# Performance work log

Hardware: AMD Instinct MI355X
Metric: run time of the kernel (lower is better)

## Reference

```python
import jax, jax.numpy as jnp
import numpy as np

BATCH, SEQ, DIM = 4, 4096, 256
DT_RANK, D_STATE, NUM_TOKENS = 16, 16, 1024


def _adapool(x, T):
    # uniform window mean == AdaptiveAvgPool1d when S % T == 0
    B, S, D = x.shape
    return x.reshape(B, T, S // T, D).mean(axis=2)


def _layernorm(x, g, b, eps=1e-5):
    mu = x.mean(-1, keepdims=True)
    var = ((x - mu) ** 2).mean(-1, keepdims=True)
    return (x - mu) * jax.lax.rsqrt(var + eps) * g + b


def _gauss_mask(T):
    c = (T + 1) // 2
    idx = jnp.arange(T, dtype=jnp.float32)
    sigma = jnp.abs(idx - c).mean()
    w = jnp.exp(-0.5 * (idx - c) ** 2 / sigma ** 2)
    return w / w.sum()


def _ssm(x, Wdbc, Wdt, bdt, Alog, D):
    A = -jnp.exp(Alog)                                     # (Dm, N)
    dbc = x @ Wdbc.T                                       # (B,L,dt+2N)
    delta = jax.nn.softplus(dbc[..., :DT_RANK] @ Wdt.T + bdt)   # (B,L,Dm)
    Bm = dbc[..., DT_RANK:DT_RANK + D_STATE]               # (B,L,N)
    Cm = dbc[..., DT_RANK + D_STATE:]                      # (B,L,N)
    deltaA = jnp.exp(delta[..., None] * A)                 # (B,L,Dm,N)
    BX = (delta[..., None] * Bm[:, :, None, :]) * x[..., None]
    def comb(c1, c2):
        a1, x1 = c1
        a2, x2 = c2
        return (a2 * a1, a2 * x1 + x2)
    _, hs = jax.lax.associative_scan(comb, (deltaA, BX), axis=1)
    y = jnp.einsum('bldn,bln->bld', hs, Cm) + D * x
    return y


def setup_inputs():
    key = jax.random.key(0)
    ks = jax.random.split(key, 16)
    s = 0.05
    Alog = jnp.tile(jnp.log(jnp.arange(1.0, D_STATE + 1.0, dtype=jnp.float32))[None, :], (DIM, 1))
    return {
        'x': jax.random.normal(ks[0], (BATCH, SEQ, DIM), jnp.float32),
        'ln_g': jnp.ones((DIM,), jnp.float32),
        'ln_b': jnp.zeros((DIM,), jnp.float32),
        'W1': jax.random.normal(ks[1], (DIM, DIM), jnp.float32) * s,
        'b1': jnp.zeros((DIM,), jnp.float32),
        'W2': jax.random.normal(ks[2], (DIM, DIM), jnp.float32) * s,
        'b2': jnp.zeros((DIM,), jnp.float32),
        'Wcf': jax.random.normal(ks[3], (DIM, DIM), jnp.float32) * s,
        'bcf': jnp.zeros((DIM,), jnp.float32),
        'Wcb': jax.random.normal(ks[4], (DIM, DIM), jnp.float32) * s,
        'bcb': jnp.zeros((DIM,), jnp.float32),
        'Wdbc_f': jax.random.normal(ks[5], (DT_RANK + 2 * D_STATE, DIM), jnp.float32) * s,
        'Wdt_f': jax.random.normal(ks[6], (DIM, DT_RANK), jnp.float32) * s,
        'bdt_f': jnp.zeros((DIM,), jnp.float32),
        'Alog_f': Alog,
        'D_f': jnp.ones((DIM,), jnp.float32),
        'Wdbc_b': jax.random.normal(ks[7], (DT_RANK + 2 * D_STATE, DIM), jnp.float32) * s,
        'Wdt_b': jax.random.normal(ks[8], (DIM, DT_RANK), jnp.float32) * s,
        'bdt_b': jnp.zeros((DIM,), jnp.float32),
        'Alog_b': Alog,
        'D_b': jnp.ones((DIM,), jnp.float32),
    }


def reference(x, ln_g, ln_b, W1, b1, W2, b2, Wcf, bcf, Wcb, bcb,
              Wdbc_f, Wdt_f, bdt_f, Alog_f, D_f,
              Wdbc_b, Wdt_b, bdt_b, Alog_b, D_b):
    skip = _adapool(x, NUM_TOKENS)
    xn = _layernorm(x, ln_g, ln_b)
    z = xn @ W1.T + b1
    xp = xn @ W2.T + b2
    mask = _gauss_mask(NUM_TOKENS)[None, :, None]

    # forward direction: 1x1 conv (= channel linear) -> softplus -> SSM
    h1 = jax.nn.softplus(jnp.einsum('bsd,ed->bse', xp, Wcf) + bcf)
    x1 = _ssm(h1, Wdbc_f, Wdt_f, bdt_f, Alog_f, D_f)
    x1 = jax.nn.silu(_adapool(x1, NUM_TOKENS) * mask)

    # backward direction on flipped sequence
    h2 = jax.nn.softplus(jnp.einsum('bsd,ed->bse', xp[:, ::-1], Wcb) + bcb)
    x2 = _ssm(h2, Wdbc_b, Wdt_b, bdt_b, Alog_b, D_b)[:, ::-1]
    x2 = jax.nn.silu(_adapool(x2, NUM_TOKENS) * mask)

    zp = jax.nn.silu(_adapool(z, NUM_TOKENS))
    return zp * x1 + zp * x2 + skip
```

## Files before the change

### kernel.cpp

```cpp
#include <hip/hip_runtime.h>
#include <math.h>


namespace {
constexpr int BB = 4;
constexpr int LL = 4096;
constexpr int DD = 256;
constexpr int NS = 16;
constexpr int NCH = 64;
constexpr int CLEN = 64;
constexpr int TOK = 1024;

constexpr size_t NROW = (size_t)BB * LL;
constexpr size_t NE   = NROW * DD;
constexpr size_t NP   = (size_t)BB * TOK * DD;
constexpr size_t NBC  = NROW * NS;
constexpr size_t NAGG = 2ull * BB * DD * NCH * NS;

constexpr size_t O_XN   = 0;
constexpr size_t O_DLF  = O_XN;
constexpr size_t O_DLB  = NE / 2;
constexpr size_t O_H1X  = NE;
constexpr size_t O_G2X  = NE + NE / 2;
constexpr size_t O_BMF  = 2 * NE;
constexpr size_t O_CMF  = O_BMF + NBC / 2;
constexpr size_t O_BMB  = O_CMF + NBC / 2;
constexpr size_t O_CMB  = O_BMB + NBC / 2;
constexpr size_t O_ZP   = O_CMB + NBC / 2;
constexpr size_t O_SKIP = O_ZP + NP;
constexpr size_t O_Y1   = O_SKIP + NP;
constexpr size_t O_Y2   = O_Y1 + NP;
constexpr size_t O_WF1  = O_Y2 + NP;
constexpr size_t O_BF1  = O_WF1 + 768 * 256 / 2;
constexpr size_t O_WF2F = O_BF1 + 768;
constexpr size_t O_B2F  = O_WF2F + 384 * 256 / 2;
constexpr size_t O_WF2B = O_B2F + 384;
constexpr size_t O_B2B  = O_WF2B + 384 * 256 / 2;
constexpr size_t O_APROD = O_B2B + 384;
constexpr size_t O_HEND = O_APROD + NAGG;
constexpr size_t O_MASK = O_HEND + NAGG;

constexpr int SSTRIDE = 136;
}

typedef __bf16 bf16x8 __attribute__((ext_vector_type(8)));
typedef float f32x4 __attribute__((ext_vector_type(4)));

__device__ __forceinline__ float softplusf(float x) {
    return fmaxf(x, 0.f) + __logf(1.f + __expf(-fabsf(x)));
}
__device__ __forceinline__ float siluf(float x) {
    return x / (1.f + __expf(-x));
}
__device__ __forceinline__ void gl_lds16(const void* g, void* l) {
    __builtin_amdgcn_global_load_lds((const __attribute__((address_space(1))) unsigned int*)g,
                                     (__attribute__((address_space(3))) unsigned int*)l, 16, 0, 0);
}
__device__ __forceinline__ void pow_chain(float e1, float* p) {
    p[0] = e1;
    p[1] = e1 * e1;
    p[2] = p[1] * e1;
    p[3] = p[1] * p[1];
    p[4] = p[3] * p[0];
    p[5] = p[3] * p[1];
    p[6] = p[3] * p[2];
    p[7] = p[3] * p[3];
    p[8]  = p[7] * p[0];
    p[9]  = p[7] * p[1];
    p[10] = p[7] * p[2];
    p[11] = p[7] * p[3];
    p[12] = p[7] * p[4];
    p[13] = p[7] * p[5];
    p[14] = p[7] * p[6];
    p[15] = p[7] * p[7];
}

__global__ __launch_bounds__(256) void prep_all_kernel(
    const float* __restrict__ W1, const float* __restrict__ b1,
    const float* __restrict__ W2, const float* __restrict__ b2,
    const float* __restrict__ Wcf, const float* __restrict__ bcf,
    const float* __restrict__ Wcb, const float* __restrict__ bcb,
    const float* __restrict__ Wdt_f, const float* __restrict__ Wdbc_f, const float* __restrict__ bdt_f,
    const float* __restrict__ Wdt_b, const float* __restrict__ Wdbc_b, const float* __restrict__ bdt_b,
    __bf16* __restrict__ Wf1, float* __restrict__ bf1,
    __bf16* __restrict__ Wf2f, float* __restrict__ b2f,
    __bf16* __restrict__ Wf2b, float* __restrict__ b2b,
    float* __restrict__ mask)
{
    int bx = blockIdx.x, mat = blockIdx.y, k = threadIdx.x;
    if (bx < 256) {
        int j = bx;
        const float* Wc = mat ? Wcb : Wcf;
        float acc = 0.f, accb = 0.f;
        for (int m = 0; m < 256; ++m) {
            float w = Wc[j * 256 + m];
            acc  = fmaf(w, W2[m * 256 + k], acc);
            accb = fmaf(w, b2[m], accb);
        }
        Wf1[(size_t)(256 + mat * 256 + j) * 256 + k] = (__bf16)acc;
        if (k == 0) bf1[256 + mat * 256 + j] = accb + (mat ? bcb[j] : bcf[j]);
        if (mat == 0) {
            Wf1[(size_t)j * 256 + k] = (__bf16)W1[j * 256 + k];
            if (k == 0) bf1[j] = b1[j];
        }
    } else if (bx < 640) {
        int j = bx - 256;
        const float* Wdt  = mat ? Wdt_b : Wdt_f;
        const float* Wdbc = mat ? Wdbc_b : Wdbc_f;
        const float* bdt  = mat ? bdt_b : bdt_f;
        __bf16* Wf2 = mat ? Wf2b : Wf2f;
        float* b2x  = mat ? b2b : b2f;
        float val;
        if (j < 256) {
            float acc = 0.f;
#pragma unroll
            for (int m = 0; m < 16; ++m)
                acc = fmaf(Wdt[j * 16 + m], Wdbc[m * 256 + k], acc);
            val = acc;
        } else if (j < 288) {
            val = Wdbc[(16 + (j - 256)) * 256 + k];
        } else {
            val = 0.f;
        }
        Wf2[(size_t)j * 256 + k] = (__bf16)val;
        if (k == 0) b2x[j] = (j < 256) ? bdt[j] : 0.f;
    } else if (mat == 0) {
        __shared__ float red[4];
        __shared__ float sb;
        float w[4];
        float loc = 0.f;
#pragma unroll
        for (int q = 0; q < 4; ++q) {
            float dd = (float)(k + 256 * q) - 512.f;
            w[q] = __expf(-0.5f * dd * dd * (1.f / 65536.f));
            loc += w[q];
        }
        for (int o = 32; o > 0; o >>= 1) loc += __shfl_xor(loc, o, 64);
        if ((k & 63) == 0) red[k >> 6] = loc;
        __syncthreads();
        if (k == 0) sb = red[0] + red[1] + red[2] + red[3];
        __syncthreads();
        float inv = 1.f / sb;
#pragma unroll
        for (int q = 0; q < 4; ++q) mask[k + 256 * q] = w[q] * inv;
    }
}

__global__ __launch_bounds__(256) void ln_kernel(
    const float* __restrict__ x, const float* __restrict__ lng, const float* __restrict__ lnb,
    __bf16* __restrict__ xn, float* __restrict__ skipo)
{
    __shared__ float red[8];
    __shared__ float mv[2];
    int t = threadIdx.x;
    int r0 = blockIdx.x * 4;
    float gg = lng[t], bbv = lnb[t];
    float acc = 0.f;
    for (int i = 0; i < 4; ++i) {
        size_t r = r0 + i;
        float v = x[r * 256 + t];
        float s = v, q = v * v;
        for (int o = 32; o > 0; o >>= 1) { s += __shfl_xor(s, o, 64); q += __shfl_xor(q, o, 64); }
        if ((t & 63) == 0) { red[t >> 6] = s; red[4 + (t >> 6)] = q; }
        __syncthreads();
        if (t == 0) {
            float S = red[0] + red[1] + red[2] + red[3];
            float Q = red[4] + red[5] + red[6] + red[7];
            float mu = S * (1.f / 256.f);
            mv[0] = mu;
            mv[1] = rsqrtf(Q * (1.f / 256.f) - mu * mu + 1e-5f);
        }
        __syncthreads();
        xn[r * 256 + t] = (__bf16)((v - mv[0]) * mv[1] * gg + bbv);
        acc += v;
        __syncthreads();
    }
    int b = r0 >> 12;
    int g = (r0 & 4095) >> 2;
    skipo[((size_t)b * TOK + g) * 256 + t] = acc * 0.25f;
}

__global__ __launch_bounds__(256) void gemm1_mfma(
    const __bf16* __restrict__ A, const __bf16* __restrict__ Bw, const float* __restrict__ bias,
    float* __restrict__ zp, __bf16* __restrict__ h1x, __bf16* __restrict__ g2x)
{
    __shared__ __align__(16) __bf16 As[4096];
    __shared__ __align__(16) __bf16 Bs[4096];
    __shared__ __align__(16) unsigned char Stage[128 * SSTRIDE * 2];
    int tid = threadIdx.x;
    int lane = tid & 63, wv = tid >> 6;
    int wr = wv >> 1, wc = wv & 1;
    int lm = lane & 15, lq = lane >> 4;
    int m0 = blockIdx.x << 7, n0 = blockIdx.y << 7;

    const __bf16* ga0 = A  + (size_t)(m0 + wv * 32 + lm) * 256 + lq * 8;
    const __bf16* ga1 = ga0 + 16 * 256;
    const __bf16* gb0 = Bw + (size_t)(n0 + wv * 32 + lm) * 256 + lq * 8;
    const __bf16* gb1 = gb0 + 16 * 256;
    __bf16* la0 = &As[(wv * 2    ) * 512];
    __bf16* la1 = &As[(wv * 2 + 1) * 512];
    __bf16* lb0 = &Bs[(wv * 2    ) * 512];
    __bf16* lb1 = &Bs[(wv * 2 + 1) * 512];

    f32x4 acc[4][4];
#pragma unroll
    for (int i = 0; i < 4; ++i)
#pragma unroll
        for (int j = 0; j < 4; ++j) acc[i][j] = 0;

    for (int k0 = 0; k0 < 256; k0 += 32) {
        __syncthreads();
        gl_lds16(ga0 + k0, la0);
        gl_lds16(ga1 + k0, la1);
        gl_lds16(gb0 + k0, lb0);
        gl_lds16(gb1 + k0, lb1);
        __syncthreads();
        bf16x8 af[4], bfr[4];
#pragma unroll
        for (int i = 0; i < 4; ++i)
            af[i] = *(const bf16x8*)&As[(wr * 4 + i) * 512 + lane * 8];
#pragma unroll
        for (int j = 0; j < 4; ++j)
            bfr[j] = *(const bf16x8*)&Bs[(wc * 4 + j) * 512 + lane * 8];
#pragma unroll
        for (int i = 0; i < 4; ++i)
#pragma unroll
            for (int j = 0; j < 4; ++j)
                acc[i][j] = __builtin_amdgcn_mfma_f32_16x16x32_bf16(af[i], bfr[j], acc[i][j], 0, 0, 0);
    }

    int target = blockIdx.y >> 1;
    int colbase = (blockIdx.y & 1) * 128;
    __syncthreads();
    if (target == 0) {
        float* zs = (float*)Stage;
#pragma unroll
        for (int j = 0; j < 4; ++j) {
            int coll = wc * 64 + j * 16 + lm;
            float bv = bias[n0 + coll];
#pragma unroll
            for (int i = 0; i < 4; ++i) {
                int gl = wr * 16 + i * 4 + lq;
                float s = acc[i][j][0] + acc[i][j][1] + acc[i][j][2] + acc[i][j][3];
                zs[gl * 132 + coll] = siluf(0.25f * s + bv);
            }
        }
        __syncthreads();
        int b = m0 >> 12, g0 = (m0 & 4095) >> 2;
        int rl = tid >> 5;
        int c4 = (tid & 31) * 4;
#pragma unroll
        for (int p = 0; p < 4; ++p) {
            int g = p * 8 + rl;
            float4 v = *(float4*)&zs[g * 132 + c4];
            *(float4*)&zp[((size_t)b * TOK + g0 + g) * 256 + colbase + c4] = v;
        }
    } else {
        __bf16* hs = (__bf16*)Stage;
#pragma unroll
        for (int j = 0; j < 4; ++j) {
            int coll = wc * 64 + j * 16 + lm;
            float bv = bias[n0 + coll];
#pragma unroll
            for (int i = 0; i < 4; ++i) {
                int rl = wr * 64 + i * 16 + lq * 4;
#pragma unroll
                for (int r = 0; r < 4; ++r)
                    hs[(rl + r) * SSTRIDE + coll] = (__bf16)softplusf(acc[i][j][r] + bv);
            }
        }
        __syncthreads();
        __bf16* outp = (target == 1) ? h1x : g2x;
        int rl = tid >> 4;
        int c8 = (tid & 15) * 8;
#pragma unroll
        for (int p = 0; p < 8; ++p) {
            int row = p * 16 + rl;
            bf16x8 v = *(bf16x8*)&hs[row * SSTRIDE + c8];
            *(bf16x8*)&outp[(size_t)(m0 + row) * 256 + colbase + c8] = v;
        }
    }
}

__global__ __launch_bounds__(256) void gemm2_mfma(
    const __bf16* __restrict__ h1x, const __bf16* __restrict__ g2x,
    const __bf16* __restrict__ Wf, const float* __restrict__ bf2,
    const __bf16* __restrict__ Wb, const float* __restrict__ bb2,
    __bf16* __restrict__ dlf, __bf16* __restrict__ dlb,
    __bf16* __restrict__ BmF, __bf16* __restrict__ CmF,
    __bf16* __restrict__ BmB, __bf16* __restrict__ CmB)
{
    __shared__ __align__(16) __bf16 As[4096];
    __shared__ __align__(16) __bf16 Bs[4096];
    __shared__ __align__(16) unsigned char Stage[128 * SSTRIDE * 2];
    int tid = threadIdx.x;
    int lane = tid & 63, wv = tid >> 6;
    int wr = wv >> 1, wc = wv & 1;
    int lm = lane & 15, lq = lane >> 4;
    int m0 = blockIdx.x << 7, n0 = blockIdx.y << 7;
    int dir = blockIdx.z;
    const __bf16* A    = dir ? g2x : h1x;
    const __bf16* Bw   = dir ? Wb : Wf;
    const float* bias  = dir ? bb2 : bf2;
    __bf16* dl = dir ? dlb : dlf;
    __bf16* Bm = dir ? BmB : BmF;
    __bf16* Cm = dir ? CmB : CmF;

    const __bf16* ga0 = A  + (size_t)(m0 + wv * 32 + lm) * 256 + lq * 8;
    const __bf16* ga1 = ga0 + 16 * 256;
    const __bf16* gb0 = Bw + (size_t)(n0 + wv * 32 + lm) * 256 + lq * 8;
    const __bf16* gb1 = gb0 + 16 * 256;
    __bf16* la0 = &As[(wv * 2    ) * 512];
    __bf16* la1 = &As[(wv * 2 + 1) * 512];
    __bf16* lb0 = &Bs[(wv * 2    ) * 512];
    __bf16* lb1 = &Bs[(wv * 2 + 1) * 512];

    f32x4 acc[4][4];
#pragma unroll
    for (int i = 0; i < 4; ++i)
#pragma unroll
        for (int j = 0; j < 4; ++j) acc[i][j] = 0;

    for (int k0 = 0; k0 < 256; k0 += 32) {
        __syncthreads();
        gl_lds16(ga0 + k0, la0);
        gl_lds16(ga1 + k0, la1);
        gl_lds16(gb0 + k0, lb0);
        gl_lds16(gb1 + k0, lb1);
        __syncthreads();
        bf16x8 af[4], bfr[4];
#pragma unroll
        for (int i = 0; i < 4; ++i)
            af[i] = *(const bf16x8*)&As[(wr * 4 + i) * 512 + lane * 8];
#pragma unroll
        for (int j = 0; j < 4; ++j)
            bfr[j] = *(const bf16x8*)&Bs[(wc * 4 + j) * 512 + lane * 8];
#pragma unroll
        for (int i = 0; i < 4; ++i)
#pragma unroll
            for (int j = 0; j < 4; ++j)
                acc[i][j] = __builtin_amdgcn_mfma_f32_16x16x32_bf16(af[i], bfr[j], acc[i][j], 0, 0, 0);
    }

    __syncthreads();
    if (blockIdx.y < 2) {
        __bf16* hs = (__bf16*)Stage;
        int colbase = (blockIdx.y & 1) * 128;
#pragma unroll
        for (int j = 0; j < 4; ++j) {
            int coll = wc * 64 + j * 16 + lm;
            float bv = bias[n0 + coll];
#pragma unroll
            for (int i = 0; i < 4; ++i) {
                int rl = wr * 64 + i * 16 + lq * 4;
#pragma unroll
                for (int r = 0; r < 4; ++r)
                    hs[(rl + r) * SSTRIDE + coll] = (__bf16)softplusf(acc[i][j][r] + bv);
            }
        }
        __syncthreads();
        int rl = tid >> 4;
        int c8 = (tid & 15) * 8;
#pragma unroll
        for (int p = 0; p < 8; ++p) {
            int row = p * 16 + rl;
            bf16x8 v = *(bf16x8*)&hs[row * SSTRIDE + c8];
            *(bf16x8*)&dl[(size_t)(m0 + row) * 256 + colbase + c8] = v;
        }
    } else {
        __bf16* bs_ = (__bf16*)Stage;
        __bf16* cs_ = (__bf16*)Stage + 128 * 24;
        if (wc == 0) {
#pragma unroll
            for (int j = 0; j < 2; ++j) {
                int coll = j * 16 + lm;
                float bv = bias[n0 + coll];
                __bf16* dst = j ? cs_ : bs_;
#pragma unroll
                for (int i = 0; i < 4; ++i) {
                    int rl = wr * 64 + i * 16 + lq * 4;
#pragma unroll
                    for (int r = 0; r < 4; ++r)
                        dst[(rl + r) * 24 + lm] = (__bf16)(acc[i][j][r] + bv);
                }
            }
        }
        __syncthreads();
        int row = tid >> 1;
        int c8 = (tid & 1) * 8;
        bf16x8 vb = *(bf16x8*)&bs_[row * 24 + c8];
        bf16x8 vc = *(bf16x8*)&cs_[row * 24 + c8];
        *(bf16x8*)&Bm[(size_t)(m0 + row) * 16 + c8] = vb;
        *(bf16x8*)&Cm[(size_t)(m0 + row) * 16 + c8] = vc;
    }
}

__global__ __launch_bounds__(256) void scan1_kernel(
    const __bf16* __restrict__ df, const __bf16* __restrict__ db,
    const __bf16* __restrict__ xf, const __bf16* __restrict__ xb,
    const __bf16* __restrict__ bmf, const __bf16* __restrict__ bmb,
    const float* __restrict__ alogf, const float* __restrict__ alogb,
    float* __restrict__ aprod, float* __restrict__ hend)
{
    int d = threadIdx.x;
    int c = blockIdx.x, b = blockIdx.y, dir = blockIdx.z;
    const __bf16* delta = dir ? db : df;
    const __bf16* xin   = dir ? xb : xf;
    const __bf16* Bm    = dir ? bmb : bmf;
    const float* Alog   = dir ? alogb : alogf;

    float A[16];
    bool intOK = true;
#pragma unroll
    for (int n = 0; n < 16; ++n) {
        A[n] = -__expf(Alog[(size_t)d * 16 + n]);
        intOK = intOK && (fabsf(A[n] + (float)(n + 1)) < 1e-3f);
    }
    float h[16];
#pragma unroll
    for (int n = 0; n < 16; ++n) h[n] = 0.f;
    float sd = 0.f;
    int base = c * CLEN;
    if (intOK) {
        for (int it = 0; it < CLEN; ++it) {
            int t = dir ? (base + CLEN - 1 - it) : (base + it);
            size_t row = (size_t)b * LL + t;
            float dlt = (float)delta[row * DD + d];
            float xv  = (float)xin[row * DD + d];
            float common = dlt * xv;
            sd += dlt;
            float p[16];
            pow_chain(__expf(-dlt), p);
            const bf16x8* Bp = (const bf16x8*)&Bm[row * NS];
            bf16x8 b0 = Bp[0], b1 = Bp[1];
#pragma unroll
            for (int n = 0; n < 8; ++n) {
                h[n]     = fmaf(p[n],     h[n],     common * (float)b0[n]);
                h[n + 8] = fmaf(p[n + 8], h[n + 8], common * (float)b1[n]);
            }
        }
        float pe[16];
        pow_chain(__expf(-sd), pe);
        size_t idx = ((((size_t)dir * BB + b) * DD + d) * NCH + c) * NS;
#pragma unroll
        for (int q = 0; q < 4; ++q) {
            float4 av, hv;
            av.x = pe[q * 4 + 0]; av.y = pe[q * 4 + 1]; av.z = pe[q * 4 + 2]; av.w = pe[q * 4 + 3];
            hv.x = h[q * 4 + 0];  hv.y = h[q * 4 + 1];  hv.z = h[q * 4 + 2];  hv.w = h[q * 4 + 3];
            *(float4*)&aprod[idx + q * 4] = av;
            *(float4*)&hend[idx + q * 4] = hv;
        }
    } else {
        for (int it = 0; it < CLEN; ++it) {
            int t = dir ? (base + CLEN - 1 - it) : (base + it);
            size_t row = (size_t)b * LL + t;
            float dlt = (float)delta[row * DD + d];
            float xv  = (float)xin[row * DD + d];
            float common = dlt * xv;
            sd += dlt;
            const bf16x8* Bp = (const bf16x8*)&Bm[row * NS];
            bf16x8 b0 = Bp[0], b1 = Bp[1];
#pragma unroll
            for (int n = 0; n < 8; ++n) {
                h[n]     = fmaf(__expf(dlt * A[n]),     h[n],     common * (float)b0[n]);
                h[n + 8] = fmaf(__expf(dlt * A[n + 8]), h[n + 8], common * (float)b1[n]);
            }
        }
        size_t idx = ((((size_t)dir * BB + b) * DD + d) * NCH + c) * NS;
#pragma unroll
        for (int n = 0; n < 16; ++n) {
            aprod[idx + n] = __expf(sd * A[n]);
            hend[idx + n] = h[n];
        }
    }
}

__global__ __launch_bounds__(256) void scan2_kernel(
    const float* __restrict__ aprod, float* __restrict__ hh)
{
    int g = blockIdx.x * 256 + threadIdx.x;
    int n = g & 15, d = (g >> 4) & 255, b = (g >> 12) & 3, dir = (g >> 14) & 1;
    size_t bidx = (((size_t)dir * BB + b) * DD + d) * NCH;
    float s = 0.f;
    if (!dir) {
#pragma unroll 8
        for (int c = 0; c < NCH; ++c) {
            size_t idx = (bidx + c) * NS + n;
            float a = aprod[idx], he = hh[idx];
            hh[idx] = s;
            s = fmaf(a, s, he);
        }
    } else {
#pragma unroll 8
        for (int c = NCH - 1; c >= 0; --c) {
            size_t idx = (bidx + c) * NS + n;
            float a = aprod[idx], he = hh[idx];
            hh[idx] = s;
            s = fmaf(a, s, he);
        }
    }
}

__global__ __launch_bounds__(256) void scan3_kernel(
    const __bf16* __restrict__ df, const __bf16* __restrict__ db,
    const __bf16* __restrict__ xf, const __bf16* __restrict__ xb,
    const __bf16* __restrict__ bmf, const __bf16* __restrict__ bmb,
    const __bf16* __restrict__ cmf, const __bf16* __restrict__ cmb,
    const float* __restrict__ alogf, const float* __restrict__ alogb,
    const float* __restrict__ Dfp, const float* __restrict__ Dbp,
    const float* __restrict__ hin,
    float* __restrict__ y1, float* __restrict__ y2)
{
    int d = threadIdx.x;
    int c = blockIdx.x, b = blockIdx.y, dir = blockIdx.z;
    const __bf16* delta = dir ? db : df;
    const __bf16* xin   = dir ? xb : xf;
    const __bf16* Bm    = dir ? bmb : bmf;
    const __bf16* Cm    = dir ? cmb : cmf;
    const float* Alog   = dir ? alogb : alogf;
    const float* Dv     = dir ? Dbp : Dfp;
    float* yout = dir ? y2 : y1;

    float A[16];
    bool intOK = true;
#pragma unroll
    for (int n = 0; n < 16; ++n) {
        A[n] = -__expf(Alog[(size_t)d * 16 + n]);
        intOK = intOK && (fabsf(A[n] + (float)(n + 1)) < 1e-3f);
    }
    float Dd = Dv[d];
    float h[16];
    size_t idx = ((((size_t)dir * BB + b) * DD + d) * NCH + c) * NS;
#pragma unroll
    for (int q = 0; q < 4; ++q) {
        float4 hv = *(const float4*)&hin[idx + q * 4];
        h[q * 4 + 0] = hv.x; h[q * 4 + 1] = hv.y; h[q * 4 + 2] = hv.z; h[q * 4 + 3] = hv.w;
    }
    int base = c * CLEN;
    float pool = 0.f;
    if (intOK) {
        for (int it = 0; it < CLEN; ++it) {
            int t = dir ? (base + CLEN - 1 - it) : (base + it);
            size_t row = (size_t)b * LL + t;
            float dlt = (float)delta[row * DD + d];
            float xv  = (float)xin[row * DD + d];
            float common = dlt * xv;
            float p[16];
            pow_chain(__expf(-dlt), p);
            const bf16x8* Bp = (const bf16x8*)&Bm[row * NS];
            const bf16x8* Cp = (const bf16x8*)&Cm[row * NS];
            bf16x8 b0 = Bp[0], b1 = Bp[1];
            bf16x8 c0 = Cp[0], c1 = Cp[1];
            float yac = 0.f;
#pragma unroll
            for (int n = 0; n < 8; ++n) {
                h[n]     = fmaf(p[n],     h[n],     common * (float)b0[n]);
                h[n + 8] = fmaf(p[n + 8], h[n + 8], common * (float)b1[n]);
                yac = fmaf(h[n], (float)c0[n], yac);
                yac = fmaf(h[n + 8], (float)c1[n], yac);
            }
            pool += yac + Dd * xv;
            bool gend = dir ? ((t & 3) == 0) : ((t & 3) == 3);
            if (gend) {
                yout[((size_t)b * TOK + (t >> 2)) * DD + d] = pool * 0.25f;
                pool = 0.f;
            }
        }
    } else {
        for (int it = 0; it < CLEN; ++it) {
            int t = dir ? (base + CLEN - 1 - it) : (base + it);
            size_t row = (size_t)b * LL + t;
            float dlt = (float)delta[row * DD + d];
            float xv  = (float)xin[row * DD + d];
            float common = dlt * xv;
            const bf16x8* Bp = (const bf16x8*)&Bm[row * NS];
            const bf16x8* Cp = (const bf16x8*)&Cm[row * NS];
            bf16x8 b0 = Bp[0], b1 = Bp[1];
            bf16x8 c0 = Cp[0], c1 = Cp[1];
            float yac = 0.f;
#pragma unroll
            for (int n = 0; n < 8; ++n) {
                h[n]     = fmaf(__expf(dlt * A[n]),     h[n],     common * (float)b0[n]);
                h[n + 8] = fmaf(__expf(dlt * A[n + 8]), h[n + 8], common * (float)b1[n]);
                yac = fmaf(h[n], (float)c0[n], yac);
                yac = fmaf(h[n + 8], (float)c1[n], yac);
            }
            pool += yac + Dd * xv;
            bool gend = dir ? ((t & 3) == 0) : ((t & 3) == 3);
            if (gend) {
                yout[((size_t)b * TOK + (t >> 2)) * DD + d] = pool * 0.25f;
                pool = 0.f;
            }
        }
    }
}

__global__ __launch_bounds__(256) void final_kernel(
    const float* __restrict__ zp, const float* __restrict__ y1, const float* __restrict__ y2,
    const float* __restrict__ mask, const float* __restrict__ skipi, float* __restrict__ out)
{
    int p = blockIdx.x;
    int g = p & 1023;
    int d = threadIdx.x;
    size_t ip = (size_t)p * 256 + d;
    float mk = mask[g];
    float a1 = y1[ip] * mk, a2 = y2[ip] * mk;
    out[ip] = zp[ip] * (siluf(a1) + siluf(a2)) + skipi[ip];
}

extern "C" void kernel_launch(void* const* d_in, const int* in_sizes, int n_in,
                              void* d_out, int out_size, void* d_ws, size_t ws_size,
                              hipStream_t stream)
{
    const float* x      = (const float*)d_in[0];
    const float* ln_g   = (const float*)d_in[1];
    const float* ln_b   = (const float*)d_in[2];
    const float* W1     = (const float*)d_in[3];
    const float* b1     = (const float*)d_in[4];
    const float* W2     = (const float*)d_in[5];
    const float* b2     = (const float*)d_in[6];
    const float* Wcf    = (const float*)d_in[7];
    const float* bcf    = (const float*)d_in[8];
    const float* Wcb    = (const float*)d_in[9];
    const float* bcb    = (const float*)d_in[10];
    const float* Wdbc_f = (const float*)d_in[11];
    const float* Wdt_f  = (const float*)d_in[12];
    const float* bdt_f  = (const float*)d_in[13];
    const float* Alog_f = (const float*)d_in[14];
    const float* D_f    = (const float*)d_in[15];
    const float* Wdbc_b = (const float*)d_in[16];
    const float* Wdt_b  = (const float*)d_in[17];
    const float* bdt_b  = (const float*)d_in[18];
    const float* Alog_b = (const float*)d_in[19];
    const float* D_b    = (const float*)d_in[20];
    float* out = (float*)d_out;
    float* ws  = (float*)d_ws;

    __bf16* xnb = (__bf16*)(ws + O_XN);
    __bf16* dlf = (__bf16*)(ws + O_DLF);
    __bf16* dlb = (__bf16*)(ws + O_DLB);
    __bf16* h1x = (__bf16*)(ws + O_H1X);
    __bf16* g2x = (__bf16*)(ws + O_G2X);
    __bf16* bmf = (__bf16*)(ws + O_BMF);
    __bf16* cmf = (__bf16*)(ws + O_CMF);
    __bf16* bmb = (__bf16*)(ws + O_BMB);
    __bf16* cmb = (__bf16*)(ws + O_CMB);
    float* zpb  = ws + O_ZP;
    float* skb  = ws + O_SKIP;
    float* y1b  = ws + O_Y1;
    float* y2b  = ws + O_Y2;
    __bf16* wf1 = (__bf16*)(ws + O_WF1);
    float* bf1  = ws + O_BF1;
    __bf16* wf2f = (__bf16*)(ws + O_WF2F);
    float* b2f  = ws + O_B2F;
    __bf16* wf2b = (__bf16*)(ws + O_WF2B);
    float* b2b  = ws + O_B2B;
    float* apr  = ws + O_APROD;
    float* hnd  = ws + O_HEND;
    float* mkb  = ws + O_MASK;

    prep_all_kernel<<<dim3(641, 2), 256, 0, stream>>>(
        W1, b1, W2, b2, Wcf, bcf, Wcb, bcb,
        Wdt_f, Wdbc_f, bdt_f, Wdt_b, Wdbc_b, bdt_b,
        wf1, bf1, wf2f, b2f, wf2b, b2b, mkb);
    ln_kernel<<<4096, 256, 0, stream>>>(x, ln_g, ln_b, xnb, skb);
    gemm1_mfma<<<dim3(128, 6), 256, 0, stream>>>(xnb, wf1, bf1, zpb, h1x, g2x);
    gemm2_mfma<<<dim3(128, 3, 2), 256, 0, stream>>>(h1x, g2x, wf2f, b2f, wf2b, b2b,
                                                    dlf, dlb, bmf, cmf, bmb, cmb);
    scan1_kernel<<<dim3(NCH, BB, 2), 256, 0, stream>>>(dlf, dlb, h1x, g2x, bmf, bmb,
                                                       Alog_f, Alog_b, apr, hnd);
    scan2_kernel<<<128, 256, 0, stream>>>(apr, hnd);
    scan3_kernel<<<dim3(NCH, BB, 2), 256, 0, stream>>>(dlf, dlb, h1x, g2x, bmf, bmb, cmf, cmb,
                                                       Alog_f, Alog_b, D_f, D_b, hnd, y1b, y2b);
    final_kernel<<<4096, 256, 0, stream>>>(zpb, y1b, y2b, mkb, skb, out);
}
```

Baseline: 243.0 us.

## Store delta and conv activations channel-major so scans read contiguous vectors

The GEMM epilogues now also write transposed (channel-major, time-contiguous) copies of the softplus conv activations and delta. This lets the scan kernels load 8 timesteps per thread in one 16-byte vector instead of a strided scalar bf16 load per timestep. LayerNorm is restructured to reduce all four rows with a single pair of barriers, and a prep loop gets an unroll pragma. The cost is extra global writes and strided LDS gathers in the GEMM epilogues, plus a larger workspace.

```diff
diff --git a/kernel.cpp b/kernel.cpp
--- a/kernel.cpp
+++ b/kernel.cpp
@@ -17,12 +17,14 @@
 constexpr size_t NBC  = NROW * NS;
 constexpr size_t NAGG = 2ull * BB * DD * NCH * NS;
 
-constexpr size_t O_XN   = 0;
-constexpr size_t O_DLF  = O_XN;
-constexpr size_t O_DLB  = NE / 2;
-constexpr size_t O_H1X  = NE;
-constexpr size_t O_G2X  = NE + NE / 2;
-constexpr size_t O_BMF  = 2 * NE;
+constexpr size_t O_H1X  = 0;
+constexpr size_t O_G2X  = NE / 2;
+constexpr size_t O_H1T  = NE;
+constexpr size_t O_G2T  = NE + NE / 2;
+constexpr size_t O_DLTF = 2 * NE;
+constexpr size_t O_XN   = O_DLTF;
+constexpr size_t O_DLTB = 2 * NE + NE / 2;
+constexpr size_t O_BMF  = 3 * NE;
 constexpr size_t O_CMF  = O_BMF + NBC / 2;
 constexpr size_t O_BMB  = O_CMF + NBC / 2;
 constexpr size_t O_CMB  = O_BMB + NBC / 2;
@@ -40,10 +42,11 @@
 constexpr size_t O_HEND = O_APROD + NAGG;
 constexpr size_t O_MASK = O_HEND + NAGG;
 
-constexpr int SSTRIDE = 136;
+constexpr int SS = 132;
 }
 
 typedef __bf16 bf16x8 __attribute__((ext_vector_type(8)));
+typedef __bf16 bf16x4 __attribute__((ext_vector_type(4)));
 typedef float f32x4 __attribute__((ext_vector_type(4)));
 
 __device__ __forceinline__ float softplusf(float x) {
@@ -92,6 +95,7 @@
         int j = bx;
         const float* Wc = mat ? Wcb : Wcf;
         float acc = 0.f, accb = 0.f;
+#pragma unroll 8
         for (int m = 0; m < 256; ++m) {
             float w = Wc[j * 256 + m];
             acc  = fmaf(w, W2[m * 256 + k], acc);
@@ -150,30 +154,44 @@
     const float* __restrict__ x, const float* __restrict__ lng, const float* __restrict__ lnb,
     __bf16* __restrict__ xn, float* __restrict__ skipo)
 {
-    __shared__ float red[8];
-    __shared__ float mv[2];
+    __shared__ float red[32];
+    __shared__ float mv[8];
     int t = threadIdx.x;
     int r0 = blockIdx.x * 4;
     float gg = lng[t], bbv = lnb[t];
+    float v[4], s[4], q[4];
+#pragma unroll
+    for (int i = 0; i < 4; ++i) {
+        v[i] = x[(size_t)(r0 + i) * 256 + t];
+        s[i] = v[i];
+        q[i] = v[i] * v[i];
+    }
+    for (int o = 32; o > 0; o >>= 1) {
+#pragma unroll
+        for (int i = 0; i < 4; ++i) {
+            s[i] += __shfl_xor(s[i], o, 64);
+            q[i] += __shfl_xor(q[i], o, 64);
+        }
+    }
+    if ((t & 63) == 0) {
+        int w = t >> 6;
+#pragma unroll
+        for (int i = 0; i < 4; ++i) { red[i * 4 + w] = s[i]; red[16 + i * 4 + w] = q[i]; }
+    }
+    __syncthreads();
+    if (t < 4) {
+        float S = red[t * 4 + 0] + red[t * 4 + 1] + red[t * 4 + 2] + red[t * 4 + 3];
+        float Q = red[16 + t * 4 + 0] + red[16 + t * 4 + 1] + red[16 + t * 4 + 2] + red[16 + t * 4 + 3];
+        float mu = S * (1.f / 256.f);
+        mv[t * 2] = mu;
+        mv[t * 2 + 1] = rsqrtf(Q * (1.f / 256.f) - mu * mu + 1e-5f);
+    }
+    __syncthreads();
     float acc = 0.f;
+#pragma unroll
     for (int i = 0; i < 4; ++i) {
-        size_t r = r0 + i;
-        float v = x[r * 256 + t];
-        float s = v, q = v * v;
-        for (int o = 32; o > 0; o >>= 1) { s += __shfl_xor(s, o, 64); q += __shfl_xor(q, o, 64); }
-        if ((t & 63) == 0) { red[t >> 6] = s; red[4 + (t >> 6)] = q; }
-        __syncthreads();
-        if (t == 0) {
-            float S = red[0] + red[1] + red[2] + red[3];
-            float Q = red[4] + red[5] + red[6] + red[7];
-            float mu = S * (1.f / 256.f);
-            mv[0] = mu;
-            mv[1] = rsqrtf(Q * (1.f / 256.f) - mu * mu + 1e-5f);
-        }
-        __syncthreads();
-        xn[r * 256 + t] = (__bf16)((v - mv[0]) * mv[1] * gg + bbv);
-        acc += v;
-        __syncthreads();
+        xn[(size_t)(r0 + i) * 256 + t] = (__bf16)((v[i] - mv[i * 2]) * mv[i * 2 + 1] * gg + bbv);
+        acc += v[i];
     }
     int b = r0 >> 12;
     int g = (r0 & 4095) >> 2;
@@ -182,11 +200,12 @@
 
 __global__ __launch_bounds__(256) void gemm1_mfma(
     const __bf16* __restrict__ A, const __bf16* __restrict__ Bw, const float* __restrict__ bias,
-    float* __restrict__ zp, __bf16* __restrict__ h1x, __bf16* __restrict__ g2x)
-{
-    __shared__ __align__(16) __bf16 As[4096];
-    __shared__ __align__(16) __bf16 Bs[4096];
-    __shared__ __align__(16) unsigned char Stage[128 * SSTRIDE * 2];
+    float* __restrict__ zp, __bf16* __restrict__ h1x, __bf16* __restrict__ g2x,
+    __bf16* __restrict__ h1T, __bf16* __restrict__ g2T)
+{
+    __shared__ __align__(16) __bf16 SH[128 * SS];
+    __bf16* As = SH;
+    __bf16* Bs = SH + 4096;
     int tid = threadIdx.x;
     int lane = tid & 63, wv = tid >> 6;
     int wr = wv >> 1, wc = wv & 1;
@@ -233,7 +252,7 @@
     int colbase = (blockIdx.y & 1) * 128;
     __syncthreads();
     if (target == 0) {
-        float* zs = (float*)Stage;
+        float* zs = (float*)SH;
 #pragma unroll
         for (int j = 0; j < 4; ++j) {
             int coll = wc * 64 + j * 16 + lm;
@@ -242,7 +261,7 @@
             for (int i = 0; i < 4; ++i) {
                 int gl = wr * 16 + i * 4 + lq;
                 float s = acc[i][j][0] + acc[i][j][1] + acc[i][j][2] + acc[i][j][3];
-                zs[gl * 132 + coll] = siluf(0.25f * s + bv);
+                zs[gl * SS + coll] = siluf(0.25f * s + bv);
             }
         }
         __syncthreads();
@@ -252,11 +271,11 @@
 #pragma unroll
         for (int p = 0; p < 4; ++p) {
             int g = p * 8 + rl;
-            float4 v = *(float4*)&zs[g * 132 + c4];
+            float4 v = *(float4*)&zs[g * SS + c4];
             *(float4*)&zp[((size_t)b * TOK + g0 + g) * 256 + colbase + c4] = v;
         }
     } else {
-        __bf16* hs = (__bf16*)Stage;
+        __bf16* hs = SH;
 #pragma unroll
         for (int j = 0; j < 4; ++j) {
             int coll = wc * 64 + j * 16 + lm;
@@ -266,18 +285,37 @@
                 int rl = wr * 64 + i * 16 + lq * 4;
 #pragma unroll
                 for (int r = 0; r < 4; ++r)
-                    hs[(rl + r) * SSTRIDE + coll] = (__bf16)softplusf(acc[i][j][r] + bv);
+                    hs[(rl + r) * SS + coll] = (__bf16)softplusf(acc[i][j][r] + bv);
             }
         }
         __syncthreads();
         __bf16* outp = (target == 1) ? h1x : g2x;
-        int rl = tid >> 4;
-        int c8 = (tid & 15) * 8;
-#pragma unroll
-        for (int p = 0; p < 8; ++p) {
-            int row = p * 16 + rl;
-            bf16x8 v = *(bf16x8*)&hs[row * SSTRIDE + c8];
-            *(bf16x8*)&outp[(size_t)(m0 + row) * 256 + colbase + c8] = v;
+        __bf16* outT = (target == 1) ? h1T : g2T;
+        {
+            int rl = tid >> 4;
+            int c8 = (tid & 15) * 8;
+#pragma unroll
+            for (int p = 0; p < 8; ++p) {
+                int row = p * 16 + rl;
+                bf16x4 lo = *(const bf16x4*)&hs[row * SS + c8];
+                bf16x4 hi = *(const bf16x4*)&hs[row * SS + c8 + 4];
+                bf16x8 v;
+#pragma unroll
+                for (int e = 0; e < 4; ++e) { v[e] = lo[e]; v[4 + e] = hi[e]; }
+                *(bf16x8*)&outp[(size_t)(m0 + row) * 256 + colbase + c8] = v;
+            }
+        }
+        {
+#pragma unroll
+            for (int it = 0; it < 8; ++it) {
+                int item = it * 256 + tid;
+                int dl_ = item & 127;
+                int tg = item >> 7;
+                bf16x8 v;
+#pragma unroll
+                for (int e = 0; e < 8; ++e) v[e] = hs[(tg * 8 + e) * SS + dl_];
+                *(bf16x8*)&outT[(size_t)(colbase + dl_) * 16384 + m0 + tg * 8] = v;
+            }
         }
     }
 }
@@ -286,13 +324,13 @@
     const __bf16* __restrict__ h1x, const __bf16* __restrict__ g2x,
     const __bf16* __restrict__ Wf, const float* __restrict__ bf2,
     const __bf16* __restrict__ Wb, const float* __restrict__ bb2,
-    __bf16* __restrict__ dlf, __bf16* __restrict__ dlb,
+    __bf16* __restrict__ dTf, __bf16* __restrict__ dTb,
     __bf16* __restrict__ BmF, __bf16* __restrict__ CmF,
     __bf16* __restrict__ BmB, __bf16* __restrict__ CmB)
 {
-    __shared__ __align__(16) __bf16 As[4096];
-    __shared__ __align__(16) __bf16 Bs[4096];
-    __shared__ __align__(16) unsigned char Stage[128 * SSTRIDE * 2];
+    __shared__ __align__(16) __bf16 SH[128 * SS];
+    __bf16* As = SH;
+    __bf16* Bs = SH + 4096;
     int tid = threadIdx.x;
     int lane = tid & 63, wv = tid >> 6;
     int wr = wv >> 1, wc = wv & 1;
@@ -302,7 +340,7 @@
     const __bf16* A    = dir ? g2x : h1x;
     const __bf16* Bw   = dir ? Wb : Wf;
     const float* bias  = dir ? bb2 : bf2;
-    __bf16* dl = dir ? dlb : dlf;
+    __bf16* dT = dir ? dTb : dTf;
     __bf16* Bm = dir ? BmB : BmF;
     __bf16* Cm = dir ? CmB : CmF;
 
@@ -344,8 +382,8 @@
 
     __syncthreads();
     if (blockIdx.y < 2) {
-        __bf16* hs = (__bf16*)Stage;
-        int colbase = (blockIdx.y & 1) * 128;
+        __bf16* hs = SH;
+        int colbase = blockIdx.y * 128;
 #pragma unroll
         for (int j = 0; j < 4; ++j) {
             int coll = wc * 64 + j * 16 + lm;
@@ -355,21 +393,23 @@
                 int rl = wr * 64 + i * 16 + lq * 4;
 #pragma unroll
                 for (int r = 0; r < 4; ++r)
-                    hs[(rl + r) * SSTRIDE + coll] = (__bf16)softplusf(acc[i][j][r] + bv);
-            }
-        }
-        __syncthreads();
-        int rl = tid >> 4;
-        int c8 = (tid & 15) * 8;
-#pragma unroll
-        for (int p = 0; p < 8; ++p) {
-            int row = p * 16 + rl;
-            bf16x8 v = *(bf16x8*)&hs[row * SSTRIDE + c8];
-            *(bf16x8*)&dl[(size_t)(m0 + row) * 256 + colbase + c8] = v;
+                    hs[(rl + r) * SS + coll] = (__bf16)softplusf(acc[i][j][r] + bv);
+            }
+        }
+        __syncthreads();
+#pragma unroll
+        for (int it = 0; it < 8; ++it) {
+            int item = it * 256 + tid;
+            int dl_ = item & 127;
+            int tg = item >> 7;
+            bf16x8 v;
+#pragma unroll
+            for (int e = 0; e < 8; ++e) v[e] = hs[(tg * 8 + e) * SS + dl_];
+            *(bf16x8*)&dT[(size_t)(colbase + dl_) * 16384 + m0 + tg * 8] = v;
         }
     } else {
-        __bf16* bs_ = (__bf16*)Stage;
-        __bf16* cs_ = (__bf16*)Stage + 128 * 24;
+        __bf16* bs_ = SH;
+        __bf16* cs_ = SH + 128 * 24;
         if (wc == 0) {
 #pragma unroll
             for (int j = 0; j < 2; ++j) {
@@ -396,18 +436,18 @@
 }
 
 __global__ __launch_bounds__(256) void scan1_kernel(
-    const __bf16* __restrict__ df, const __bf16* __restrict__ db,
-    const __bf16* __restrict__ xf, const __bf16* __restrict__ xb,
+    const __bf16* __restrict__ dTf, const __bf16* __restrict__ dTb,
+    const __bf16* __restrict__ xTf, const __bf16* __restrict__ xTb,
     const __bf16* __restrict__ bmf, const __bf16* __restrict__ bmb,
     const float* __restrict__ alogf, const float* __restrict__ alogb,
     float* __restrict__ aprod, float* __restrict__ hend)
 {
     int d = threadIdx.x;
     int c = blockIdx.x, b = blockIdx.y, dir = blockIdx.z;
-    const __bf16* delta = dir ? db : df;
-    const __bf16* xin   = dir ? xb : xf;
-    const __bf16* Bm    = dir ? bmb : bmf;
-    const float* Alog   = dir ? alogb : alogf;
+    const __bf16* dT = dir ? dTb : dTf;
+    const __bf16* xT = dir ? xTb : xTf;
+    const __bf16* Bm = dir ? bmb : bmf;
+    const float* Alog = dir ? alogb : alogf;
 
     float A[16];
     bool intOK = true;
@@ -420,23 +460,29 @@
 #pragma unroll
     for (int n = 0; n < 16; ++n) h[n] = 0.f;
     float sd = 0.f;
-    int base = c * CLEN;
+    size_t tb = (size_t)d * 16384 + (size_t)b * 4096 + (size_t)c * CLEN;
+    size_t rowb = (size_t)b * LL + (size_t)c * CLEN;
     if (intOK) {
-        for (int it = 0; it < CLEN; ++it) {
-            int t = dir ? (base + CLEN - 1 - it) : (base + it);
-            size_t row = (size_t)b * LL + t;
-            float dlt = (float)delta[row * DD + d];
-            float xv  = (float)xin[row * DD + d];
-            float common = dlt * xv;
-            sd += dlt;
-            float p[16];
-            pow_chain(__expf(-dlt), p);
-            const bf16x8* Bp = (const bf16x8*)&Bm[row * NS];
-            bf16x8 b0 = Bp[0], b1 = Bp[1];
-#pragma unroll
-            for (int n = 0; n < 8; ++n) {
-                h[n]     = fmaf(p[n],     h[n],     common * (float)b0[n]);
-                h[n + 8] = fmaf(p[n + 8], h[n + 8], common * (float)b1[n]);
+        for (int g = 0; g < 8; ++g) {
+            int tblk = dir ? (56 - 8 * g) : 8 * g;
+            bf16x8 dv = *(const bf16x8*)&dT[tb + tblk];
+            bf16x8 xv8 = *(const bf16x8*)&xT[tb + tblk];
+#pragma unroll
+            for (int ii = 0; ii < 8; ++ii) {
+                int i = dir ? (7 - ii) : ii;
+                float dlt = (float)dv[i];
+                float xv  = (float)xv8[i];
+                float common = dlt * xv;
+                sd += dlt;
+                float p[16];
+                pow_chain(__expf(-dlt), p);
+                const bf16x8* Bp = (const bf16x8*)&Bm[(rowb + tblk + i) * NS];
+                bf16x8 b0 = Bp[0], b1 = Bp[1];
+#pragma unroll
+                for (int n = 0; n < 8; ++n) {
+                    h[n]     = fmaf(p[n],     h[n],     common * (float)b0[n]);
+                    h[n + 8] = fmaf(p[n + 8], h[n + 8], common * (float)b1[n]);
+                }
             }
         }
         float pe[16];
@@ -451,19 +497,24 @@
             *(float4*)&hend[idx + q * 4] = hv;
         }
     } else {
-        for (int it = 0; it < CLEN; ++it) {
-            int t = dir ? (base + CLEN - 1 - it) : (base + it);
-            size_t row = (size_t)b * LL + t;
-            float dlt = (float)delta[row * DD + d];
-            float xv  = (float)xin[row * DD + d];
-            float common = dlt * xv;
-            sd += dlt;
-            const bf16x8* Bp = (const bf16x8*)&Bm[row * NS];
-            bf16x8 b0 = Bp[0], b1 = Bp[1];
-#pragma unroll
-            for (int n = 0; n < 8; ++n) {
-                h[n]     = fmaf(__expf(dlt * A[n]),     h[n],     common * (float)b0[n]);
-                h[n + 8] = fmaf(__expf(dlt * A[n + 8]), h[n + 8], common * (float)b1[n]);
+        for (int g = 0; g < 8; ++g) {
+            int tblk = dir ? (56 - 8 * g) : 8 * g;
+            bf16x8 dv = *(const bf16x8*)&dT[tb + tblk];
+            bf16x8 xv8 = *(const bf16x8*)&xT[tb + tblk];
+#pragma unroll
+            for (int ii = 0; ii < 8; ++ii) {
+                int i = dir ? (7 - ii) : ii;
+                float dlt = (float)dv[i];
+                float xv  = (float)xv8[i];
+                float common = dlt * xv;
+                sd += dlt;
+                const bf16x8* Bp = (const bf16x8*)&Bm[(rowb + tblk + i) * NS];
+                bf16x8 b0 = Bp[0], b1 = Bp[1];
+#pragma unroll
+                for (int n = 0; n < 8; ++n) {
+                    h[n]     = fmaf(__expf(dlt * A[n]),     h[n],     common * (float)b0[n]);
+                    h[n + 8] = fmaf(__expf(dlt * A[n + 8]), h[n + 8], common * (float)b1[n]);
+                }
             }
         }
         size_t idx = ((((size_t)dir * BB + b) * DD + d) * NCH + c) * NS;
@@ -502,8 +553,8 @@
 }
 
 __global__ __launch_bounds__(256) void scan3_kernel(
-    const __bf16* __restrict__ df, const __bf16* __restrict__ db,
-    const __bf16* __restrict__ xf, const __bf16* __restrict__ xb,
+    const __bf16* __restrict__ dTf, const __bf16* __restrict__ dTb,
+    const __bf16* __restrict__ xTf, const __bf16* __restrict__ xTb,
     const __bf16* __restrict__ bmf, const __bf16* __restrict__ bmb,
     const __bf16* __restrict__ cmf, const __bf16* __restrict__ cmb,
     const float* __restrict__ alogf, const float* __restrict__ alogb,
@@ -513,12 +564,12 @@
 {
     int d = threadIdx.x;
     int c = blockIdx.x, b = blockIdx.y, dir = blockIdx.z;
-    const __bf16* delta = dir ? db : df;
-    const __bf16* xin   = dir ? xb : xf;
-    const __bf16* Bm    = dir ? bmb : bmf;
-    const __bf16* Cm    = dir ? cmb : cmf;
-    const float* Alog   = dir ? alogb : alogf;
-    const float* Dv     = dir ? Dbp : Dfp;
+    const __bf16* dT = dir ? dTb : dTf;
+    const __bf16* xT = dir ? xTb : xTf;
+    const __bf16* Bm = dir ? bmb : bmf;
+    const __bf16* Cm = dir ? cmb : cmf;
+    const float* Alog = dir ? alogb : alogf;
+    const float* Dv   = dir ? Dbp : Dfp;
     float* yout = dir ? y2 : y1;
 
     float A[16];
@@ -536,60 +587,74 @@
         float4 hv = *(const float4*)&hin[idx + q * 4];
         h[q * 4 + 0] = hv.x; h[q * 4 + 1] = hv.y; h[q * 4 + 2] = hv.z; h[q * 4 + 3] = hv.w;
     }
+    size_t tb = (size_t)d * 16384 + (size_t)b * 4096 + (size_t)c * CLEN;
+    size_t rowb = (size_t)b * LL + (size_t)c * CLEN;
     int base = c * CLEN;
     float pool = 0.f;
     if (intOK) {
-        for (int it = 0; it < CLEN; ++it) {
-            int t = dir ? (base + CLEN - 1 - it) : (base + it);
-            size_t row = (size_t)b * LL + t;
-            float dlt = (float)delta[row * DD + d];
-            float xv  = (float)xin[row * DD + d];
-            float common = dlt * xv;
-            float p[16];
-            pow_chain(__expf(-dlt), p);
-            const bf16x8* Bp = (const bf16x8*)&Bm[row * NS];
-            const bf16x8* Cp = (const bf16x8*)&Cm[row * NS];
-            bf16x8 b0 = Bp[0], b1 = Bp[1];
-            bf16x8 c0 = Cp[0], c1 = Cp[1];
-            float yac = 0.f;
-#pragma unroll
-            for (int n = 0; n < 8; ++n) {
-                h[n]     = fmaf(p[n],     h[n],     common * (float)b0[n]);
-                h[n + 8] = fmaf(p[n + 8], h[n + 8], common * (float)b1[n]);
-                yac = fmaf(h[n], (float)c0[n], yac);
-                yac = fmaf(h[n + 8], (float)c1[n], yac);
-            }
-            pool += yac + Dd * xv;
-            bool gend = dir ? ((t & 3) == 0) : ((t & 3) == 3);
-            if (gend) {
-                yout[((size_t)b * TOK + (t >> 2)) * DD + d] = pool * 0.25f;
-                pool = 0.f;
+        for (int g = 0; g < 8; ++g) {
+            int tblk = dir ? (56 - 8 * g) : 8 * g;
+            bf16x8 dv = *(const bf16x8*)&dT[tb + tblk];
+            bf16x8 xv8 = *(const bf16x8*)&xT[tb + tblk];
+#pragma unroll
+            for (int ii = 0; ii < 8; ++ii) {
+                int i = dir ? (7 - ii) : ii;
+                float dlt = (float)dv[i];
+                float xv  = (float)xv8[i];
+                float common = dlt * xv;
+                float p[16];
+                pow_chain(__expf(-dlt), p);
+                const bf16x8* Bp = (const bf16x8*)&Bm[(rowb + tblk + i) * NS];
+                const bf16x8* Cp = (const bf16x8*)&Cm[(rowb + tblk + i) * NS];
+                bf16x8 b0 = Bp[0], b1 = Bp[1];
+                bf16x8 c0 = Cp[0], c1 = Cp[1];
+                float yac = 0.f;
+#pragma unroll
+                for (int n = 0; n < 8; ++n) {
+                    h[n]     = fmaf(p[n],     h[n],     common * (float)b0[n]);
+                    h[n + 8] = fmaf(p[n + 8], h[n + 8], common * (float)b1[n]);
+                    yac = fmaf(h[n], (float)c0[n], yac);
+                    yac = fmaf(h[n + 8], (float)c1[n], yac);
+                }
+                pool += yac + Dd * xv;
+                int t = base + tblk + i;
+                bool gend = dir ? ((t & 3) == 0) : ((t & 3) == 3);
+                if (gend) {
+                    yout[((size_t)b * TOK + (t >> 2)) * DD + d] = pool * 0.25f;
+                    pool = 0.f;
+                }
             }
         }
     } else {
-        for (int it = 0; it < CLEN; ++it) {
-            int t = dir ? (base + CLEN - 1 - it) : (base + it);
-            size_t row = (size_t)b * LL + t;
-            float dlt = (float)delta[row * DD + d];
-            float xv  = (float)xin[row * DD + d];
-            float common = dlt * xv;
-            const bf16x8* Bp = (const bf16x8*)&Bm[row * NS];
-            const bf16x8* Cp = (const bf16x8*)&Cm[row * NS];
-            bf16x8 b0 = Bp[0], b1 = Bp[1];
-            bf16x8 c0 = Cp[0], c1 = Cp[1];
-            float yac = 0.f;
-#pragma unroll
-            for (int n = 0; n < 8; ++n) {
-                h[n]     = fmaf(__expf(dlt * A[n]),     h[n],     common * (float)b0[n]);
-                h[n + 8] = fmaf(__expf(dlt * A[n + 8]), h[n + 8], common * (float)b1[n]);
-                yac = fmaf(h[n], (float)c0[n], yac);
-                yac = fmaf(h[n + 8], (float)c1[n], yac);
-            }
-            pool += yac + Dd * xv;
-            bool gend = dir ? ((t & 3) == 0) : ((t & 3) == 3);
-            if (gend) {
-                yout[((size_t)b * TOK + (t >> 2)) * DD + d] = pool * 0.25f;
-                pool = 0.f;
+        for (int g = 0; g < 8; ++g) {
+            int tblk = dir ? (56 - 8 * g) : 8 * g;
+            bf16x8 dv = *(const bf16x8*)&dT[tb + tblk];
+            bf16x8 xv8 = *(const bf16x8*)&xT[tb + tblk];
+#pragma unroll
+            for (int ii = 0; ii < 8; ++ii) {
+                int i = dir ? (7 - ii) : ii;
+                float dlt = (float)dv[i];
+                float xv  = (float)xv8[i];
+                float common = dlt * xv;
+                const bf16x8* Bp = (const bf16x8*)&Bm[(rowb + tblk + i) * NS];
+                const bf16x8* Cp = (const bf16x8*)&Cm[(rowb + tblk + i) * NS];
+                bf16x8 b0 = Bp[0], b1 = Bp[1];
+                bf16x8 c0 = Cp[0], c1 = Cp[1];
+                float yac = 0.f;
+#pragma unroll
+                for (int n = 0; n < 8; ++n) {
+                    h[n]     = fmaf(__expf(dlt * A[n]),     h[n],     common * (float)b0[n]);
+                    h[n + 8] = fmaf(__expf(dlt * A[n + 8]), h[n + 8], common * (float)b1[n]);
+                    yac = fmaf(h[n], (float)c0[n], yac);
+                    yac = fmaf(h[n + 8], (float)c1[n], yac);
+                }
+                pool += yac + Dd * xv;
+                int t = base + tblk + i;
+                bool gend = dir ? ((t & 3) == 0) : ((t & 3) == 3);
+                if (gend) {
+                    yout[((size_t)b * TOK + (t >> 2)) * DD + d] = pool * 0.25f;
+                    pool = 0.f;
+                }
             }
         }
     }
@@ -636,11 +701,13 @@
     float* out = (float*)d_out;
     float* ws  = (float*)d_ws;
 
-    __bf16* xnb = (__bf16*)(ws + O_XN);
-    __bf16* dlf = (__bf16*)(ws + O_DLF);
-    __bf16* dlb = (__bf16*)(ws + O_DLB);
     __bf16* h1x = (__bf16*)(ws + O_H1X);
     __bf16* g2x = (__bf16*)(ws + O_G2X);
+    __bf16* h1T = (__bf16*)(ws + O_H1T);
+    __bf16* g2T = (__bf16*)(ws + O_G2T);
+    __bf16* xnb = (__bf16*)(ws + O_XN);
+    __bf16* dTf = (__bf16*)(ws + O_DLTF);
+    __bf16* dTb = (__bf16*)(ws + O_DLTB);
     __bf16* bmf = (__bf16*)(ws + O_BMF);
     __bf16* cmf = (__bf16*)(ws + O_CMF);
     __bf16* bmb = (__bf16*)(ws + O_BMB);
@@ -664,13 +731,13 @@
         Wdt_f, Wdbc_f, bdt_f, Wdt_b, Wdbc_b, bdt_b,
         wf1, bf1, wf2f, b2f, wf2b, b2b, mkb);
     ln_kernel<<<4096, 256, 0, stream>>>(x, ln_g, ln_b, xnb, skb);
-    gemm1_mfma<<<dim3(128, 6), 256, 0, stream>>>(xnb, wf1, bf1, zpb, h1x, g2x);
+    gemm1_mfma<<<dim3(128, 6), 256, 0, stream>>>(xnb, wf1, bf1, zpb, h1x, g2x, h1T, g2T);
     gemm2_mfma<<<dim3(128, 3, 2), 256, 0, stream>>>(h1x, g2x, wf2f, b2f, wf2b, b2b,
-                                                    dlf, dlb, bmf, cmf, bmb, cmb);
-    scan1_kernel<<<dim3(NCH, BB, 2), 256, 0, stream>>>(dlf, dlb, h1x, g2x, bmf, bmb,
+                                                    dTf, dTb, bmf, cmf, bmb, cmb);
+    scan1_kernel<<<dim3(NCH, BB, 2), 256, 0, stream>>>(dTf, dTb, h1T, g2T, bmf, bmb,
                                                        Alog_f, Alog_b, apr, hnd);
     scan2_kernel<<<128, 256, 0, stream>>>(apr, hnd);
-    scan3_kernel<<<dim3(NCH, BB, 2), 256, 0, stream>>>(dlf, dlb, h1x, g2x, bmf, bmb, cmf, cmb,
+    scan3_kernel<<<dim3(NCH, BB, 2), 256, 0, stream>>>(dTf, dTb, h1T, g2T, bmf, bmb, cmf, cmb,
                                                        Alog_f, Alog_b, D_f, D_b, hnd, y1b, y2b);
     final_kernel<<<4096, 256, 0, stream>>>(zpb, y1b, y2b, mkb, skb, out);
 }
```

Result: slower. 259.0 us (+6.6%).
